# Kernel optimization log

Measured on AMD Instinct MI355X. Metric: run time of the kernel, lower is better.

The kernel has to match this reference:

```python
import jax, jax.numpy as jnp
import numpy as np

H = 512  # hidden size

def gru_cell(x, h, Wih, Whh, bih, bhh):
    # PyTorch GRU cell: gates ordered [r, z, n]
    gi = x @ Wih.T + bih          # (B, 3H)
    gh = h @ Whh.T + bhh          # (B, 3H)
    ir, iz, inn = gi[:, :H], gi[:, H:2*H], gi[:, 2*H:]
    hr, hz, hn = gh[:, :H], gh[:, H:2*H], gh[:, 2*H:]
    r = jax.nn.sigmoid(ir + hr)
    z = jax.nn.sigmoid(iz + hz)
    n = jnp.tanh(inn + r * hn)
    return (1.0 - z) * n + z * h

def setup_inputs() -> dict:
    key = jax.random.key(0)
    ks = jax.random.split(key, 12)
    S, B, V, E, OUT = 400, 128, 50000, 300, 2
    s = 0.05
    return {
        "X": jax.random.randint(ks[0], (S, B), 0, V, dtype=jnp.int32),
        "emb": jax.random.normal(ks[1], (V, E), jnp.float32),
        "Wih0": jax.random.normal(ks[2], (2, 3*H, E), jnp.float32) * s,
        "Whh0": jax.random.normal(ks[3], (2, 3*H, H), jnp.float32) * s,
        "bih0": jax.random.normal(ks[4], (2, 3*H), jnp.float32) * s,
        "bhh0": jax.random.normal(ks[5], (2, 3*H), jnp.float32) * s,
        "Wih1": jax.random.normal(ks[6], (2, 3*H, 2*H), jnp.float32) * s,
        "Whh1": jax.random.normal(ks[7], (2, 3*H, H), jnp.float32) * s,
        "bih1": jax.random.normal(ks[8], (2, 3*H), jnp.float32) * s,
        "bhh1": jax.random.normal(ks[9], (2, 3*H), jnp.float32) * s,
        "Ws": jax.random.normal(ks[10], (OUT, 2*H), jnp.float32) * s,
        "bs": jax.random.normal(ks[11], (OUT,), jnp.float32) * s,
    }

def reference(X, emb, Wih0, Whh0, bih0, bhh0, Wih1, Whh1, bih1, bhh1, Ws, bs):
    # NOTE: the original torch code feeds the bidirectional GRU one timestep
    # at a time while threading ht, so the 'reverse' direction ALSO runs
    # left-to-right (with its own weights). We reproduce exactly that.
    S, B = X.shape
    embedded = emb[X]  # (S, B, E)
    h0 = jnp.zeros((B, H), embedded.dtype)

    def step(carry, xt):
        h0f, h0b, h1f, h1b = carry
        h0f = gru_cell(xt, h0f, Wih0[0], Whh0[0], bih0[0], bhh0[0])
        h0b = gru_cell(xt, h0b, Wih0[1], Whh0[1], bih0[1], bhh0[1])
        y0 = jnp.concatenate([h0f, h0b], axis=-1)  # (B, 2H)
        h1f = gru_cell(y0, h1f, Wih1[0], Whh1[0], bih1[0], bhh1[0])
        h1b = gru_cell(y0, h1b, Wih1[1], Whh1[1], bih1[1], bhh1[1])
        return (h1f := h1f, h0b, h1f, h1b) if False else ((h0f, h0b, h1f, h1b), None)

    (h0f, h0b, h1f, h1b), _ = jax.lax.scan(step, (h0, h0, h0, h0), embedded)
    yt = jnp.concatenate([h1f, h1b], axis=-1)  # (B, 2H) last-step output
    logits = yt @ Ws.T + bs
    return jax.nn.log_softmax(logits, axis=1)
```

## Files before the change

kernel.cpp:

```cpp
#include <hip/hip_runtime.h>


typedef unsigned int u32;
typedef unsigned short u16;
typedef __attribute__((ext_vector_type(8))) _Float16 f16x8;
typedef __attribute__((ext_vector_type(4))) float f32x4;
typedef __attribute__((ext_vector_type(16))) float f32x16;
typedef __attribute__((ext_vector_type(4))) u32 u32x4;

#define AS1 __attribute__((address_space(1)))
#define AS3 __attribute__((address_space(3)))

__device__ __forceinline__ void gl_lds16(const void* g, void* l) {
  __builtin_amdgcn_global_load_lds((AS1 void*)g, (AS3 void*)l, 16, 0, 0);
}
__device__ __forceinline__ u16 f2h(float f) {
  _Float16 h = (_Float16)f;
  return __builtin_bit_cast(u16, h);
}
__device__ __forceinline__ u32 pack2(float a, float b) {
  return (u32)f2h(a) | ((u32)f2h(b) << 16);
}
__device__ __forceinline__ float sigm(float x) {
  x = fminf(fmaxf(x, -30.f), 30.f);
  return 1.f / (1.f + __expf(-x));
}
__device__ __forceinline__ float tanh_(float x) {
  x = fminf(fmaxf(x, -15.f), 15.f);
  float e = __expf(2.f * x);
  return (e - 1.f) / (e + 1.f);
}
__device__ __forceinline__ f32x16 mfma32(f16x8 a, f16x8 b, f32x16 c) {
  return __builtin_amdgcn_mfma_f32_32x32x16_f16(a, b, c, 0, 0, 0);
}
__device__ __forceinline__ f16x8 load_cc(const u16* sbase, u32 voff) {
  f16x8 r;
  asm volatile("global_load_dwordx4 %0, %1, %2 sc0 sc1"
               : "=v"(r) : "v"(voff), "s"(sbase) : "memory");
  return r;
}
__device__ __forceinline__ void store_cc16(u16* sbase, u32 voff, u32 val) {
  asm volatile("global_store_short %0, %1, %2 sc0 sc1"
               :: "v"(voff), "v"(val), "s"(sbase) : "memory");
}
__device__ __forceinline__ void wait_vm0() {
  asm volatile("s_waitcnt vmcnt(0)" ::: "memory");
}

__device__ __forceinline__ void gridbar16(unsigned* cnt, unsigned* gen) {
  __syncthreads();
  if (threadIdx.x == 0) {
    unsigned g = __hip_atomic_load(gen, __ATOMIC_RELAXED, __HIP_MEMORY_SCOPE_AGENT);
    unsigned a = __hip_atomic_fetch_add(cnt, 1u, __ATOMIC_RELAXED, __HIP_MEMORY_SCOPE_AGENT);
    if (a == 15u) {
      __hip_atomic_store(cnt, 0u, __ATOMIC_RELAXED, __HIP_MEMORY_SCOPE_AGENT);
      __hip_atomic_fetch_add(gen, 1u, __ATOMIC_RELAXED, __HIP_MEMORY_SCOPE_AGENT);
    } else {
      while (__hip_atomic_load(gen, __ATOMIC_RELAXED, __HIP_MEMORY_SCOPE_AGENT) == g)
        __builtin_amdgcn_s_sleep(1);
    }
  }
  __syncthreads();
}

__global__ __launch_bounds__(256) void pack_wih(const float* __restrict__ W,
                                                u16* __restrict__ out, int K, int Kp, int total) {
  int idx = blockIdx.x * 256 + threadIdx.x;
  if (idx >= total) return;
  int n = idx / Kp, k = idx - n * Kp;
  out[idx] = (k < K) ? f2h(W[(size_t)n * K + k]) : (u16)0;
}

__global__ __launch_bounds__(256) void pack_whh(const float* __restrict__ W,
                                                u16* __restrict__ out) {
  int idx = blockIdx.x * 256 + threadIdx.x;
  int l = idx & 63;
  int kt = (idx >> 6) & 31;
  int rest = idx >> 11;
  int g = rest % 3, dc = rest / 3;
  int d = dc >> 4, c = dc & 15;
  int row = g * 512 + c * 32 + (l & 31);
  int k0 = kt * 16 + (l >> 5) * 8;
  const float* src = W + ((size_t)d * 1536 + row) * 512 + k0;
  u32* o = (u32*)(out + (size_t)idx * 8);
#pragma unroll
  for (int e2 = 0; e2 < 4; ++e2) o[e2] = pack2(src[2 * e2], src[2 * e2 + 1]);
}

__global__ __launch_bounds__(256) void pack_bias(const float* __restrict__ bih,
                                                 const float* __restrict__ bhh,
                                                 float* __restrict__ out) {
  int idx = blockIdx.x * 256 + threadIdx.x;
  int j = idx & 511;
  int slot = (idx >> 9) & 3;
  int d = idx >> 11;
  float v;
  if (slot == 0) v = bih[d * 1536 + j] + bhh[d * 1536 + j];
  else if (slot == 1) v = bih[d * 1536 + 512 + j] + bhh[d * 1536 + 512 + j];
  else if (slot == 2) v = bih[d * 1536 + 1024 + j];
  else v = bhh[d * 1536 + 1024 + j];
  out[idx] = v;
}

__global__ __launch_bounds__(256) void gather_emb(const int* __restrict__ X,
                                                  const float* __restrict__ emb,
                                                  u32* __restrict__ out, int t0, int total) {
  int idx = blockIdx.x * 256 + threadIdx.x;
  if (idx >= total) return;
  int r = idx / 160, kp = idx - r * 160;
  int k = kp * 2;
  int tok = X[t0 * 128 + r];
  float v0 = (k < 300) ? emb[(size_t)tok * 300 + k] : 0.f;
  float v1 = (k < 299) ? emb[(size_t)tok * 300 + k + 1] : 0.f;
  out[idx] = pack2(v0, v1);
}

__global__ __launch_bounds__(256) void gemm_f16(const u16* __restrict__ A,
                                                const u16* __restrict__ B,
                                                u16* __restrict__ giP, int K) {
  __shared__ u16 As[4096];
  __shared__ u16 Bs[4096];
  const int tid = threadIdx.x;
  const int w = tid >> 6, l = tid & 63;
  const long m0 = (long)blockIdx.y << 7;
  const long n0 = (long)blockIdx.x << 7;
  const int wm = w >> 1, wn = w & 1;
  f32x4 acc[4][4] = {};

  const int srow = w * 16 + (l >> 2);
  const int scol = (l & 3) * 8;
  const u16* ga = A + (m0 + srow) * K + scol;
  const u16* gb = B + (n0 + srow) * K + scol;
  u16* lA = &As[w * 512];
  u16* lB = &Bs[w * 512];

  for (int k0 = 0; k0 < K; k0 += 32) {
    gl_lds16(ga + k0, lA);
    gl_lds16(ga + 64 * K + k0, lA + 2048);
    gl_lds16(gb + k0, lB);
    gl_lds16(gb + 64 * K + k0, lB + 2048);
    __syncthreads();
    f16x8 af[4], bf[4];
#pragma unroll
    for (int mi = 0; mi < 4; ++mi)
      af[mi] = *(const f16x8*)&As[(wm * 64 + mi * 16 + (l & 15)) * 32 + ((l >> 4) & 3) * 8];
#pragma unroll
    for (int ni = 0; ni < 4; ++ni)
      bf[ni] = *(const f16x8*)&Bs[(wn * 64 + ni * 16 + (l & 15)) * 32 + ((l >> 4) & 3) * 8];
#pragma unroll
    for (int mi = 0; mi < 4; ++mi)
#pragma unroll
      for (int ni = 0; ni < 4; ++ni)
        acc[mi][ni] = __builtin_amdgcn_mfma_f32_16x16x32_f16(af[mi], bf[ni], acc[mi][ni], 0, 0, 0);
    __syncthreads();
  }
  const int crow = wm * 64 + ((l >> 4) << 2);
  const int ccol = wn * 64 + (l & 15);
#pragma unroll
  for (int mi = 0; mi < 4; ++mi)
#pragma unroll
    for (int ni = 0; ni < 4; ++ni)
#pragma unroll
      for (int i = 0; i < 4; ++i) {
        int grow = (int)m0 + crow + mi * 16 + i;
        int col = (int)n0 + ccol + ni * 16;
        int t_rel = grow >> 7, b = grow & 127;
        int dd = (col >= 1536) ? 1 : 0;
        int cc2 = col - dd * 1536;
        int g = cc2 >> 9, ch = (cc2 >> 5) & 15, jj = cc2 & 31;
        int wt = b >> 5, reg = (b & 3) | (((b >> 3) & 3) << 2), l5 = (b >> 2) & 1;
        int lt = jj | (l5 << 5);
        int s = g * 16 + reg, n2 = s >> 3, e = s & 7;
        size_t idx = (((((size_t)t_rel * 2 + dd) * 16 + ch) * 4 + wt) * 6 + n2) * 512 + lt * 8 + e;
        giP[idx] = f2h(acc[mi][ni][i]);
      }
}

__global__ __launch_bounds__(256, 1) void gru_layer(const u16* __restrict__ gi,
                                                    const u16* __restrict__ WhhP,
                                                    const float* __restrict__ biasP,
                                                    float* __restrict__ hf,
                                                    u16* __restrict__ hp,
                                                    u16* __restrict__ y0,
                                                    int t0, int TC,
                                                    unsigned* __restrict__ bar) {
  const int bid = blockIdx.x;
  const int d = bid >> 4, c = bid & 15;
  const int tid = threadIdx.x;
  const int w = tid >> 6, l = tid & 63;

  __shared__ u16 Wl[49152];

  {
    const u32x4* src = (const u32x4*)(WhhP + (size_t)(d * 16 + c) * 49152);
    u32x4* dst = (u32x4*)Wl;
#pragma unroll
    for (int i = 0; i < 24; ++i) dst[i * 256 + tid] = src[i * 256 + tid];
  }

  const int jcol = c * 32 + (l & 31);
  const float bsr = biasP[(d * 4 + 0) * 512 + jcol];
  const float bsz = biasP[(d * 4 + 1) * 512 + jcol];
  const float bin = biasP[(d * 4 + 2) * 512 + jcol];
  const float bhn = biasP[(d * 4 + 3) * 512 + jcol];

  const int l5 = l >> 5;
  float hreg[16];
#pragma unroll
  for (int r = 0; r < 16; ++r) {
    int row = (r & 3) + 8 * (r >> 2) + 4 * l5;
    hreg[r] = hf[((size_t)d * 128 + w * 32 + row) * 512 + jcol];
  }
  __syncthreads();

  f16x8 giv[6];
  {
    const u16* gp = gi + ((((size_t)0 * 2 + d) * 16 + c) * 4 + w) * 6 * 512 + l * 8;
#pragma unroll
    for (int n2 = 0; n2 < 6; ++n2) giv[n2] = *(const f16x8*)(gp + n2 * 512);
  }
  wait_vm0();

  unsigned* cnt = bar + d * 32;
  unsigned* gen = bar + d * 32 + 16;
  const u32 aoffbase = (u32)((d * 4 + w) * 32768 + l * 16);
  const int ktj = jcol >> 4;
  const int lb5 = ((l >> 3) & 1) << 5;
  const int ej = l & 7;

  for (int t = t0; t < t0 + TC; ++t) {
    const u16* hrb = hp + (size_t)(t & 1) * 131072;
    f16x8 a[32];
#pragma unroll
    for (int kt = 0; kt < 32; ++kt) a[kt] = load_cc(hrb, aoffbase + (u32)kt * 1024u);

    f32x16 accR = {}, accZ = {}, accN = {};
#pragma unroll
    for (int g4 = 0; g4 < 8; ++g4) {
      asm volatile("s_waitcnt vmcnt(%0)" ::"n"(28 - 4 * 8 / 2) : "memory");
      break;
    }
#pragma unroll
    for (int g4 = 0; g4 < 8; ++g4) {
      switch (g4) {
        case 0: asm volatile("s_waitcnt vmcnt(28)" ::: "memory"); break;
        case 1: asm volatile("s_waitcnt vmcnt(24)" ::: "memory"); break;
        case 2: asm volatile("s_waitcnt vmcnt(20)" ::: "memory"); break;
        case 3: asm volatile("s_waitcnt vmcnt(16)" ::: "memory"); break;
        case 4: asm volatile("s_waitcnt vmcnt(12)" ::: "memory"); break;
        case 5: asm volatile("s_waitcnt vmcnt(8)" ::: "memory"); break;
        case 6: asm volatile("s_waitcnt vmcnt(4)" ::: "memory"); break;
        default: asm volatile("s_waitcnt vmcnt(0)" ::: "memory"); break;
      }
      __builtin_amdgcn_sched_barrier(0);
#pragma unroll
      for (int kk = 0; kk < 4; ++kk) {
        int kt = g4 * 4 + kk;
        f16x8 b0 = *(const f16x8*)&Wl[(0 * 32 + kt) * 512 + l * 8];
        f16x8 b1 = *(const f16x8*)&Wl[(1 * 32 + kt) * 512 + l * 8];
        f16x8 b2 = *(const f16x8*)&Wl[(2 * 32 + kt) * 512 + l * 8];
        accR = mfma32(a[kt], b0, accR);
        accZ = mfma32(a[kt], b1, accZ);
        accN = mfma32(a[kt], b2, accN);
      }
    }

    u16* hwb = hp + (size_t)((t + 1) & 1) * 131072;
#pragma unroll
    for (int r = 0; r < 16; ++r) {
      float gr = (float)giv[r >> 3][r & 7];
      float gz = (float)giv[2 + (r >> 3)][r & 7];
      float gn = (float)giv[4 + (r >> 3)][r & 7];
      float rr = sigm(gr + accR[r] + bsr);
      float zz = sigm(gz + accZ[r] + bsz);
      float nn = tanh_(gn + bin + rr * (accN[r] + bhn));
      float h = (1.f - zz) * nn + zz * hreg[r];
      hreg[r] = h;
      int row = (r & 3) + 8 * (r >> 2) + 4 * l5;
      u32 voff = (u32)(((((d * 4 + w) * 32 + ktj) * 64 + (row | lb5)) * 8 + ej) * 2);
      store_cc16(hwb, voff, (u32)f2h(h));
      if (y0) {
        int b = w * 32 + row;
        y0[((size_t)t * 128 + b) * 1024 + d * 512 + jcol] = f2h(h);
      }
    }

    wait_vm0();

    if (t + 1 < t0 + TC) {
      const u16* gp = gi + ((((size_t)(t + 1 - t0) * 2 + d) * 16 + c) * 4 + w) * 6 * 512 + l * 8;
#pragma unroll
      for (int n2 = 0; n2 < 6; ++n2) giv[n2] = *(const f16x8*)(gp + n2 * 512);
      gridbar16(cnt, gen);
    }
  }

#pragma unroll
  for (int r = 0; r < 16; ++r) {
    int row = (r & 3) + 8 * (r >> 2) + 4 * l5;
    hf[((size_t)d * 128 + w * 32 + row) * 512 + jcol] = hreg[r];
  }
  wait_vm0();
}

__global__ __launch_bounds__(128) void classify(const float* __restrict__ hf,
                                                const float* __restrict__ Ws,
                                                const float* __restrict__ bs,
                                                float* __restrict__ out) {
  int b = threadIdx.x;
  float l0 = bs[0], l1 = bs[1];
#pragma unroll 8
  for (int j = 0; j < 512; ++j) {
    float v = hf[b * 512 + j];
    l0 = fmaf(v, Ws[j], l0);
    l1 = fmaf(v, Ws[1024 + j], l1);
  }
#pragma unroll 8
  for (int j = 0; j < 512; ++j) {
    float v = hf[(128 + b) * 512 + j];
    l0 = fmaf(v, Ws[512 + j], l0);
    l1 = fmaf(v, Ws[1536 + j], l1);
  }
  float m = fmaxf(l0, l1);
  float lse = m + __logf(__expf(l0 - m) + __expf(l1 - m));
  out[b * 2] = l0 - lse;
  out[b * 2 + 1] = l1 - lse;
}

extern "C" void kernel_launch(void* const* d_in, const int* in_sizes, int n_in,
                              void* d_out, int out_size, void* d_ws, size_t ws_size,
                              hipStream_t stream) {
  const int* X = (const int*)d_in[0];
  const float* emb = (const float*)d_in[1];
  const float* Wih0 = (const float*)d_in[2];
  const float* Whh0 = (const float*)d_in[3];
  const float* bih0 = (const float*)d_in[4];
  const float* bhh0 = (const float*)d_in[5];
  const float* Wih1 = (const float*)d_in[6];
  const float* Whh1 = (const float*)d_in[7];
  const float* bih1 = (const float*)d_in[8];
  const float* bhh1 = (const float*)d_in[9];
  const float* Ws = (const float*)d_in[10];
  const float* bs = (const float*)d_in[11];
  float* out = (float*)d_out;

  const int S = 400, B = 128;
  auto need = [&](int nc) -> size_t {
    size_t TC = (size_t)S / nc, R = TC * B;
    size_t sz = 0;
    sz += R * 3072 * 2;
    sz += (size_t)S * B * 1024 * 2;
    sz += R * 320 * 2;
    sz += (size_t)3072 * 320 * 2;
    sz += (size_t)3072 * 1024 * 2;
    sz += 2 * (size_t)1572864 * 2;
    sz += 2 * (size_t)4096 * 4;
    sz += 2 * (size_t)131072 * 4;
    sz += 2 * (size_t)262144 * 2;
    sz += 65536;
    return sz;
  };
  int nc = 16;
  if (need(1) <= ws_size) nc = 1;
  else if (need(2) <= ws_size) nc = 2;
  else if (need(4) <= ws_size) nc = 4;
  else if (need(8) <= ws_size) nc = 8;
  const int TC = S / nc;
  const size_t R = (size_t)TC * B;

  char* p = (char*)d_ws;
  auto alloc = [&](size_t bytes) {
    char* q = p;
    p += (bytes + 255) & ~(size_t)255;
    return q;
  };
  u16* giPack = (u16*)alloc(R * 3072 * 2);
  u16* y0 = (u16*)alloc((size_t)S * B * 1024 * 2);
  u16* embC = (u16*)alloc(R * 320 * 2);
  u16* B0p = (u16*)alloc((size_t)3072 * 320 * 2);
  u16* B1p = (u16*)alloc((size_t)3072 * 1024 * 2);
  u16* WhhP0 = (u16*)alloc((size_t)1572864 * 2);
  u16* WhhP1 = (u16*)alloc((size_t)1572864 * 2);
  float* biasP0 = (float*)alloc(4096 * 4);
  float* biasP1 = (float*)alloc(4096 * 4);
  float* hf0 = (float*)alloc(131072 * 4);
  float* hf1 = (float*)alloc(131072 * 4);
  u16* hp0 = (u16*)alloc(262144 * 2);
  u16* hp1 = (u16*)alloc(262144 * 2);
  unsigned* bar0 = (unsigned*)alloc(256);
  unsigned* bar1 = (unsigned*)alloc(256);

  hipMemsetAsync(hf0, 0, 131072 * 4, stream);
  hipMemsetAsync(hf1, 0, 131072 * 4, stream);
  hipMemsetAsync(hp0, 0, 262144 * 2, stream);
  hipMemsetAsync(hp1, 0, 262144 * 2, stream);
  hipMemsetAsync(bar0, 0, 256, stream);
  hipMemsetAsync(bar1, 0, 256, stream);

  pack_wih<<<3840, 256, 0, stream>>>(Wih0, B0p, 300, 320, 3072 * 320);
  pack_wih<<<12288, 256, 0, stream>>>(Wih1, B1p, 1024, 1024, 3072 * 1024);
  pack_whh<<<768, 256, 0, stream>>>(Whh0, WhhP0);
  pack_whh<<<768, 256, 0, stream>>>(Whh1, WhhP1);
  pack_bias<<<16, 256, 0, stream>>>(bih0, bhh0, biasP0);
  pack_bias<<<16, 256, 0, stream>>>(bih1, bhh1, biasP1);

  dim3 gg(24, (unsigned)(R / 128));
  for (int cix = 0; cix < nc; ++cix) {
    int t0 = cix * TC;
    int total = (int)(R * 160);
    gather_emb<<<(total + 255) / 256, 256, 0, stream>>>(X, emb, (u32*)embC, t0, total);
    gemm_f16<<<gg, 256, 0, stream>>>(embC, B0p, giPack, 320);
    gru_layer<<<32, 256, 0, stream>>>(giPack, WhhP0, biasP0, hf0, hp0, y0, t0, TC, bar0);
  }
  for (int cix = 0; cix < nc; ++cix) {
    int t0 = cix * TC;
    gemm_f16<<<gg, 256, 0, stream>>>(y0 + (size_t)t0 * 128 * 1024, B1p, giPack, 1024);
    gru_layer<<<32, 256, 0, stream>>>(giPack, WhhP1, biasP1, hf1, hp1, (u16*)nullptr, t0, TC, bar1);
  }
  classify<<<1, 128, 0, stream>>>(hf1, Ws, bs, out);
}
```

Measured before the change: 7.724 ms.

## Replace atomic grid barrier with per-block step flags and 4-deep hidden ring

The counter/generation grid barrier used after each timestep is replaced by per-block flag words. Each block publishes the completed step number, and at the next step consumers poll the 16 producer flags of their direction before loading h. The hidden-state buffer grows from double to quadruple buffering, so a fast block can run ahead without overwriting state a slower block still reads. This removes the serialized atomic round trip and the sleep-polling latency on every step. It relies on correct memory ordering of the cache-bypassing flag store relative to the h stores, and it adds an extra gi prefetch on the final step.

```diff
diff --git a/kernel.cpp b/kernel.cpp
--- a/kernel.cpp
+++ b/kernel.cpp
@@ -45,22 +45,6 @@
 }
 __device__ __forceinline__ void wait_vm0() {
   asm volatile("s_waitcnt vmcnt(0)" ::: "memory");
-}
-
-__device__ __forceinline__ void gridbar16(unsigned* cnt, unsigned* gen) {
-  __syncthreads();
-  if (threadIdx.x == 0) {
-    unsigned g = __hip_atomic_load(gen, __ATOMIC_RELAXED, __HIP_MEMORY_SCOPE_AGENT);
-    unsigned a = __hip_atomic_fetch_add(cnt, 1u, __ATOMIC_RELAXED, __HIP_MEMORY_SCOPE_AGENT);
-    if (a == 15u) {
-      __hip_atomic_store(cnt, 0u, __ATOMIC_RELAXED, __HIP_MEMORY_SCOPE_AGENT);
-      __hip_atomic_fetch_add(gen, 1u, __ATOMIC_RELAXED, __HIP_MEMORY_SCOPE_AGENT);
-    } else {
-      while (__hip_atomic_load(gen, __ATOMIC_RELAXED, __HIP_MEMORY_SCOPE_AGENT) == g)
-        __builtin_amdgcn_s_sleep(1);
-    }
-  }
-  __syncthreads();
 }
 
 __global__ __launch_bounds__(256) void pack_wih(const float* __restrict__ W,
@@ -182,8 +166,8 @@
                                                     float* __restrict__ hf,
                                                     u16* __restrict__ hp,
                                                     u16* __restrict__ y0,
-                                                    int t0, int TC,
-                                                    unsigned* __restrict__ bar) {
+                                                    u32* __restrict__ flags,
+                                                    int t0, int TC) {
   const int bid = blockIdx.x;
   const int d = bid >> 4, c = bid & 15;
   const int tid = threadIdx.x;
@@ -215,31 +199,34 @@
 
   f16x8 giv[6];
   {
-    const u16* gp = gi + ((((size_t)0 * 2 + d) * 16 + c) * 4 + w) * 6 * 512 + l * 8;
+    const u16* gp = gi + (((size_t)(0 * 2 + d) * 16 + c) * 4 + w) * 3072 + l * 8;
 #pragma unroll
     for (int n2 = 0; n2 < 6; ++n2) giv[n2] = *(const f16x8*)(gp + n2 * 512);
   }
-  wait_vm0();
-
-  unsigned* cnt = bar + d * 32;
-  unsigned* gen = bar + d * 32 + 16;
+
   const u32 aoffbase = (u32)((d * 4 + w) * 32768 + l * 16);
   const int ktj = jcol >> 4;
   const int lb5 = ((l >> 3) & 1) << 5;
   const int ej = l & 7;
+  const u32 foff = (u32)((l & 15) * 4);
 
   for (int t = t0; t < t0 + TC; ++t) {
-    const u16* hrb = hp + (size_t)(t & 1) * 131072;
+    {
+      const u32* fb = flags + (size_t)(d * 4 + (t & 3)) * 16;
+      for (;;) {
+        u32 v;
+        asm volatile("global_load_dword %0, %1, %2 sc0 sc1\n\ts_waitcnt vmcnt(0)"
+                     : "=v"(v) : "v"(foff), "s"(fb) : "memory");
+        if (__all((int)(v >= (u32)t))) break;
+      }
+    }
+
+    const u16* hrb = hp + (size_t)(t & 3) * 131072;
     f16x8 a[32];
 #pragma unroll
     for (int kt = 0; kt < 32; ++kt) a[kt] = load_cc(hrb, aoffbase + (u32)kt * 1024u);
 
     f32x16 accR = {}, accZ = {}, accN = {};
-#pragma unroll
-    for (int g4 = 0; g4 < 8; ++g4) {
-      asm volatile("s_waitcnt vmcnt(%0)" ::"n"(28 - 4 * 8 / 2) : "memory");
-      break;
-    }
 #pragma unroll
     for (int g4 = 0; g4 < 8; ++g4) {
       switch (g4) {
@@ -265,7 +252,7 @@
       }
     }
 
-    u16* hwb = hp + (size_t)((t + 1) & 1) * 131072;
+    u16* hwb = hp + (size_t)((t + 1) & 3) * 131072;
 #pragma unroll
     for (int r = 0; r < 16; ++r) {
       float gr = (float)giv[r >> 3][r & 7];
@@ -285,13 +272,21 @@
       }
     }
 
-    wait_vm0();
-
-    if (t + 1 < t0 + TC) {
-      const u16* gp = gi + ((((size_t)(t + 1 - t0) * 2 + d) * 16 + c) * 4 + w) * 6 * 512 + l * 8;
+    {
+      int rel = t + 1 - t0;
+      if (rel >= TC) rel = TC - 1;
+      const u16* gp = gi + (((size_t)rel * 2 + d) * 16 + c) * 4 * 3072 + (size_t)w * 3072 + l * 8;
 #pragma unroll
       for (int n2 = 0; n2 < 6; ++n2) giv[n2] = *(const f16x8*)(gp + n2 * 512);
-      gridbar16(cnt, gen);
+    }
+
+    asm volatile("s_waitcnt vmcnt(0)" ::: "memory");
+    __syncthreads();
+    if (tid == 0) {
+      u32* fw = flags + (size_t)(d * 4 + ((t + 1) & 3)) * 16 + c;
+      u32 val = (u32)(t + 1);
+      asm volatile("global_store_dword %0, %1, %2 sc0 sc1"
+                   :: "v"(0u), "v"(val), "s"(fw) : "memory");
     }
   }
 
@@ -356,7 +351,7 @@
     sz += 2 * (size_t)1572864 * 2;
     sz += 2 * (size_t)4096 * 4;
     sz += 2 * (size_t)131072 * 4;
-    sz += 2 * (size_t)262144 * 2;
+    sz += 2 * (size_t)524288 * 2;
     sz += 65536;
     return sz;
   };
@@ -385,17 +380,17 @@
   float* biasP1 = (float*)alloc(4096 * 4);
   float* hf0 = (float*)alloc(131072 * 4);
   float* hf1 = (float*)alloc(131072 * 4);
-  u16* hp0 = (u16*)alloc(262144 * 2);
-  u16* hp1 = (u16*)alloc(262144 * 2);
-  unsigned* bar0 = (unsigned*)alloc(256);
-  unsigned* bar1 = (unsigned*)alloc(256);
+  u16* hp0 = (u16*)alloc(524288 * 2);
+  u16* hp1 = (u16*)alloc(524288 * 2);
+  u32* flags0 = (u32*)alloc(1024);
+  u32* flags1 = (u32*)alloc(1024);
 
   hipMemsetAsync(hf0, 0, 131072 * 4, stream);
   hipMemsetAsync(hf1, 0, 131072 * 4, stream);
-  hipMemsetAsync(hp0, 0, 262144 * 2, stream);
-  hipMemsetAsync(hp1, 0, 262144 * 2, stream);
-  hipMemsetAsync(bar0, 0, 256, stream);
-  hipMemsetAsync(bar1, 0, 256, stream);
+  hipMemsetAsync(hp0, 0, 524288 * 2, stream);
+  hipMemsetAsync(hp1, 0, 524288 * 2, stream);
+  hipMemsetAsync(flags0, 0, 1024, stream);
+  hipMemsetAsync(flags1, 0, 1024, stream);
 
   pack_wih<<<3840, 256, 0, stream>>>(Wih0, B0p, 300, 320, 3072 * 320);
   pack_wih<<<12288, 256, 0, stream>>>(Wih1, B1p, 1024, 1024, 3072 * 1024);
@@ -410,12 +405,12 @@
     int total = (int)(R * 160);
     gather_emb<<<(total + 255) / 256, 256, 0, stream>>>(X, emb, (u32*)embC, t0, total);
     gemm_f16<<<gg, 256, 0, stream>>>(embC, B0p, giPack, 320);
-    gru_layer<<<32, 256, 0, stream>>>(giPack, WhhP0, biasP0, hf0, hp0, y0, t0, TC, bar0);
+    gru_layer<<<32, 256, 0, stream>>>(giPack, WhhP0, biasP0, hf0, hp0, y0, flags0, t0, TC);
   }
   for (int cix = 0; cix < nc; ++cix) {
     int t0 = cix * TC;
     gemm_f16<<<gg, 256, 0, stream>>>(y0 + (size_t)t0 * 128 * 1024, B1p, giPack, 1024);
-    gru_layer<<<32, 256, 0, stream>>>(giPack, WhhP1, biasP1, hf1, hp1, (u16*)nullptr, t0, TC, bar1);
+    gru_layer<<<32, 256, 0, stream>>>(giPack, WhhP1, biasP1, hf1, hp1, (u16*)nullptr, flags1, t0, TC);
   }
   classify<<<1, 128, 0, stream>>>(hf1, Ws, bs, out);
 }
```

Measured after the change: 6.710 ms. 1.15x faster.
